# Performance work log

Hardware: AMD Instinct MI355X
Metric: run time of the kernel (lower is better)

## Reference

```python
import jax, jax.numpy as jnp
import numpy as np

NUM_ITERS = 3     # args.num_iters_sk
EPSILON = 0.05    # args.epsilon_sk
# imb_factor = 1 -> uniform row marginal r

B, K = 16384, 4096  # batch, num prototypes/classes


def setup_inputs() -> dict:
    key = jax.random.key(0)
    logits = jax.random.normal(key, (B, K), dtype=jnp.float32)
    return {"logits": logits}


def shoot_infs(x):
    # Replace infs by the max of the tensor with infs zeroed (matches torch helper)
    mask = jnp.isinf(x)
    tmp = jnp.where(mask, jnp.zeros((), x.dtype), x)
    m = jnp.max(tmp)
    return jnp.where(mask, m, tmp)


def reference(logits):
    q = logits / EPSILON
    q = q - jnp.max(q)          # global max for numerical stability
    Q = jnp.exp(q).T            # [K, B]
    Q = shoot_infs(Q)
    Q = Q / jnp.sum(Q)
    k, b = Q.shape
    r = jnp.full((k,), 1.0 / k, dtype=Q.dtype)  # uniform class marginal (imb_factor == 1)
    c = jnp.full((b,), 1.0 / b, dtype=Q.dtype)  # uniform sample marginal
    for _ in range(NUM_ITERS):
        u = r / jnp.sum(Q, axis=1)
        u = shoot_infs(u)
        Q = Q * u[:, None]
        Q = Q * (c / jnp.sum(Q, axis=0))[None, :]
    return (Q / jnp.sum(Q, axis=0, keepdims=True)).T.astype(jnp.float32)  # [B, K]
```

## Files before the change

### kernel.cpp

```cpp
#include <hip/hip_runtime.h>
#include <hip/hip_bf16.h>
#include <math.h>

#define EPS_INV 20.0f
#define B_ROWS 16384
#define K_COLS 4096

__device__ __forceinline__ unsigned enc_f(float f) {
  unsigned u = __float_as_uint(f);
  return (u & 0x80000000u) ? ~u : (u | 0x80000000u);
}
__device__ __forceinline__ float dec_f(unsigned u) {
  u = (u & 0x80000000u) ? (u ^ 0x80000000u) : ~u;
  return __uint_as_float(u);
}

__global__ void k_max(const float4* __restrict__ x, unsigned* __restrict__ gmax, int n4) {
  int tid = blockIdx.x * blockDim.x + threadIdx.x;
  int stride = gridDim.x * blockDim.x;
  float m = -3.4e38f;
  for (int i = tid; i < n4; i += stride) {
    float4 v = x[i];
    m = fmaxf(m, fmaxf(fmaxf(v.x, v.y), fmaxf(v.z, v.w)));
  }
  #pragma unroll
  for (int off = 32; off > 0; off >>= 1)
    m = fmaxf(m, __shfl_xor(m, off, 64));
  if ((threadIdx.x & 63) == 0) atomicMax(gmax, enc_f(m));
}

__global__ void k_colsum(const float* __restrict__ logits,
                         const unsigned* __restrict__ gmaxp,
                         const float* __restrict__ beta,
                         float* __restrict__ T, int rows_per_block) {
  float m = dec_f(*gmaxp);
  int c0 = blockIdx.x * 1024 + threadIdx.x * 4;
  int r0 = blockIdx.y * rows_per_block;
  float4 acc = make_float4(0.f, 0.f, 0.f, 0.f);
  for (int r = r0; r < r0 + rows_per_block; ++r) {
    float w = beta ? beta[r] : 1.0f;
    float4 v = *(const float4*)(logits + (size_t)r * K_COLS + c0);
    acc.x += w * __expf((v.x - m) * EPS_INV);
    acc.y += w * __expf((v.y - m) * EPS_INV);
    acc.z += w * __expf((v.z - m) * EPS_INV);
    acc.w += w * __expf((v.w - m) * EPS_INV);
  }
  atomicAdd(T + c0 + 0, acc.x);
  atomicAdd(T + c0 + 1, acc.y);
  atomicAdd(T + c0 + 2, acc.z);
  atomicAdd(T + c0 + 3, acc.w);
}

__global__ void k_alpha1(const float* __restrict__ T0, float* __restrict__ alpha) {
  __shared__ float sred[4];
  int tid = threadIdx.x;
  float s = 0.f;
  for (int i = tid; i < K_COLS; i += 256) s += T0[i];
  #pragma unroll
  for (int off = 32; off > 0; off >>= 1) s += __shfl_xor(s, off, 64);
  if ((tid & 63) == 0) sred[tid >> 6] = s;
  __syncthreads();
  float S = sred[0] + sred[1] + sred[2] + sred[3];
  float c = S * (1.0f / (float)K_COLS);
  for (int i = tid; i < K_COLS; i += 256) alpha[i] = c / T0[i];
}

__global__ void k_alpha_from_T(const float* __restrict__ T, float* __restrict__ alpha) {
  int i = blockIdx.x * blockDim.x + threadIdx.x;
  if (i < K_COLS) alpha[i] = (1.0f / (float)K_COLS) / T[i];
}

__global__ void k_rowsum_beta(const float* __restrict__ logits,
                              const unsigned* __restrict__ gmaxp,
                              const float* __restrict__ alpha,
                              float* __restrict__ beta) {
  float m = dec_f(*gmaxp);
  int lane = threadIdx.x & 63;
  int r = blockIdx.x * 4 + (threadIdx.x >> 6);
  const float4* row = (const float4*)(logits + (size_t)r * K_COLS);
  const float4* a4 = (const float4*)alpha;
  float acc = 0.f;
  #pragma unroll
  for (int j = 0; j < 16; ++j) {
    int i = lane + j * 64;
    float4 v = row[i];
    float4 a = a4[i];
    acc += a.x * __expf((v.x - m) * EPS_INV)
         + a.y * __expf((v.y - m) * EPS_INV)
         + a.z * __expf((v.z - m) * EPS_INV)
         + a.w * __expf((v.w - m) * EPS_INV);
  }
  #pragma unroll
  for (int off = 32; off > 0; off >>= 1) acc += __shfl_xor(acc, off, 64);
  if (lane == 0) beta[r] = (1.0f / (float)B_ROWS) / acc;
}

__global__ void k_finalize(const float* __restrict__ logits,
                           const unsigned* __restrict__ gmaxp,
                           const float* __restrict__ alpha,
                           float4* __restrict__ out) {
  float m = dec_f(*gmaxp);
  int lane = threadIdx.x & 63;
  int r = blockIdx.x * 4 + (threadIdx.x >> 6);
  const float4* row = (const float4*)(logits + (size_t)r * K_COLS);
  const float4* a4 = (const float4*)alpha;
  float4 prod[16];
  float acc = 0.f;
  #pragma unroll
  for (int j = 0; j < 16; ++j) {
    int i = lane + j * 64;
    float4 v = row[i];
    float4 a = a4[i];
    float4 p;
    p.x = a.x * __expf((v.x - m) * EPS_INV);
    p.y = a.y * __expf((v.y - m) * EPS_INV);
    p.z = a.z * __expf((v.z - m) * EPS_INV);
    p.w = a.w * __expf((v.w - m) * EPS_INV);
    prod[j] = p;
    acc += p.x + p.y + p.z + p.w;
  }
  #pragma unroll
  for (int off = 32; off > 0; off >>= 1) acc += __shfl_xor(acc, off, 64);
  float inv = 1.0f / acc;
  float4* orow = out + (size_t)r * (K_COLS / 4);
  #pragma unroll
  for (int j = 0; j < 16; ++j) {
    int i = lane + j * 64;
    float4 p = prod[j];
    p.x *= inv; p.y *= inv; p.z *= inv; p.w *= inv;
    orow[i] = p;
  }
}

extern "C" void kernel_launch(void* const* d_in, const int* in_sizes, int n_in,
                              void* d_out, int out_size, void* d_ws, size_t ws_size,
                              hipStream_t stream) {
  const float* logits = (const float*)d_in[0];
  char* ws = (char*)d_ws;

  unsigned* gmax = (unsigned*)ws;
  float* T0    = (float*)(ws + 1024);
  float* T1    = T0 + K_COLS;
  float* T2    = T1 + K_COLS;
  float* alpha = T2 + K_COLS;
  float* beta  = alpha + K_COLS;

  hipMemsetAsync(d_ws, 0, 1024 + 3 * K_COLS * sizeof(float), stream);

  const int n4 = (B_ROWS * K_COLS) / 4;
  k_max<<<2048, 256, 0, stream>>>((const float4*)logits, gmax, n4);

  dim3 cs_grid(4, 256);
  k_colsum<<<cs_grid, 256, 0, stream>>>(logits, gmax, nullptr, T0, 64);
  k_alpha1<<<1, 256, 0, stream>>>(T0, alpha);

  k_rowsum_beta<<<B_ROWS / 4, 256, 0, stream>>>(logits, gmax, alpha, beta);
  k_colsum<<<cs_grid, 256, 0, stream>>>(logits, gmax, beta, T1, 64);
  k_alpha_from_T<<<K_COLS / 256, 256, 0, stream>>>(T1, alpha);

  k_rowsum_beta<<<B_ROWS / 4, 256, 0, stream>>>(logits, gmax, alpha, beta);
  k_colsum<<<cs_grid, 256, 0, stream>>>(logits, gmax, beta, T2, 64);
  k_alpha_from_T<<<K_COLS / 256, 256, 0, stream>>>(T2, alpha);

  k_finalize<<<B_ROWS / 4, 256, 0, stream>>>(logits, gmax, alpha, (float4*)d_out);
}
```

Baseline: 792.6 us.

## Cache exp values as bf16 and fuse row/column Sinkhorn passes

The first column-sum pass now also writes exp((x-m)/eps) as a bf16 matrix into the workspace. Later Sinkhorn iterations read that half-size matrix instead of recomputing exp from the fp32 logits, which cuts memory traffic and transcendental work. The rowsum and beta-weighted colsum are fused into one kernel that accumulates column sums in shared memory, removing one full pass per iteration. The max kernel is unrolled with more loads in flight. Rounding the intermediates to bf16 lowers accuracy, and the fast path needs a 128MB workspace, otherwise it falls back to fused fp32 kernels.

New measurement: 1.379 ms. 74.0% more time.

```diff
diff --git a/kernel.cpp b/kernel.cpp
--- a/kernel.cpp
+++ b/kernel.cpp
@@ -5,6 +5,7 @@
 #define EPS_INV 20.0f
 #define B_ROWS 16384
 #define K_COLS 4096
+#define N4     ((B_ROWS * (size_t)K_COLS) / 4)
 
 __device__ __forceinline__ unsigned enc_f(float f) {
   unsigned u = __float_as_uint(f);
@@ -15,40 +16,61 @@
   return __uint_as_float(u);
 }
 
-__global__ void k_max(const float4* __restrict__ x, unsigned* __restrict__ gmax, int n4) {
-  int tid = blockIdx.x * blockDim.x + threadIdx.x;
-  int stride = gridDim.x * blockDim.x;
+__device__ __forceinline__ unsigned short f2bf(float f) {
+  unsigned u = __float_as_uint(f);
+  return (unsigned short)((u + 0x7FFFu + ((u >> 16) & 1u)) >> 16);
+}
+__device__ __forceinline__ float bf_lo(unsigned w) { return __uint_as_float(w << 16); }
+__device__ __forceinline__ float bf_hi(unsigned w) { return __uint_as_float(w & 0xFFFF0000u); }
+
+__global__ __launch_bounds__(256) void k_max(const float4* __restrict__ x,
+                                             unsigned* __restrict__ gmax) {
+  const int tid = blockIdx.x * 256 + threadIdx.x;
+  const int nth = 1024 * 256;
   float m = -3.4e38f;
-  for (int i = tid; i < n4; i += stride) {
-    float4 v = x[i];
-    m = fmaxf(m, fmaxf(fmaxf(v.x, v.y), fmaxf(v.z, v.w)));
-  }
-  #pragma unroll
-  for (int off = 32; off > 0; off >>= 1)
-    m = fmaxf(m, __shfl_xor(m, off, 64));
+  for (int it = 0; it < 8; ++it) {
+    float4 v[8];
+    #pragma unroll
+    for (int j = 0; j < 8; ++j) v[j] = x[(size_t)tid + (size_t)(it * 8 + j) * nth];
+    #pragma unroll
+    for (int j = 0; j < 8; ++j)
+      m = fmaxf(m, fmaxf(fmaxf(v[j].x, v[j].y), fmaxf(v[j].z, v[j].w)));
+  }
+  #pragma unroll
+  for (int off = 32; off > 0; off >>= 1) m = fmaxf(m, __shfl_xor(m, off, 64));
   if ((threadIdx.x & 63) == 0) atomicMax(gmax, enc_f(m));
 }
 
-__global__ void k_colsum(const float* __restrict__ logits,
-                         const unsigned* __restrict__ gmaxp,
-                         const float* __restrict__ beta,
-                         float* __restrict__ T, int rows_per_block) {
-  float m = dec_f(*gmaxp);
-  int c0 = blockIdx.x * 1024 + threadIdx.x * 4;
-  int r0 = blockIdx.y * rows_per_block;
+__global__ __launch_bounds__(256) void k_exp_colsum(const float* __restrict__ logits,
+                                                    const unsigned* __restrict__ gmaxp,
+                                                    unsigned short* __restrict__ E,
+                                                    float* __restrict__ T0) {
+  const float m = dec_f(*gmaxp);
+  const int c0 = blockIdx.x * 1024 + threadIdx.x * 4;
+  const int r0 = blockIdx.y * 64;
   float4 acc = make_float4(0.f, 0.f, 0.f, 0.f);
-  for (int r = r0; r < r0 + rows_per_block; ++r) {
-    float w = beta ? beta[r] : 1.0f;
-    float4 v = *(const float4*)(logits + (size_t)r * K_COLS + c0);
-    acc.x += w * __expf((v.x - m) * EPS_INV);
-    acc.y += w * __expf((v.y - m) * EPS_INV);
-    acc.z += w * __expf((v.z - m) * EPS_INV);
-    acc.w += w * __expf((v.w - m) * EPS_INV);
-  }
-  atomicAdd(T + c0 + 0, acc.x);
-  atomicAdd(T + c0 + 1, acc.y);
-  atomicAdd(T + c0 + 2, acc.z);
-  atomicAdd(T + c0 + 3, acc.w);
+  for (int rr = 0; rr < 64; rr += 4) {
+    float4 v[4];
+    #pragma unroll
+    for (int j = 0; j < 4; ++j)
+      v[j] = *(const float4*)(logits + (size_t)(r0 + rr + j) * K_COLS + c0);
+    #pragma unroll
+    for (int j = 0; j < 4; ++j) {
+      float e0 = __expf((v[j].x - m) * EPS_INV);
+      float e1 = __expf((v[j].y - m) * EPS_INV);
+      float e2 = __expf((v[j].z - m) * EPS_INV);
+      float e3 = __expf((v[j].w - m) * EPS_INV);
+      acc.x += e0; acc.y += e1; acc.z += e2; acc.w += e3;
+      if (E) {
+        ushort4 w = make_ushort4(f2bf(e0), f2bf(e1), f2bf(e2), f2bf(e3));
+        *(ushort4*)(E + (size_t)(r0 + rr + j) * K_COLS + c0) = w;
+      }
+    }
+  }
+  atomicAdd(T0 + c0 + 0, acc.x);
+  atomicAdd(T0 + c0 + 1, acc.y);
+  atomicAdd(T0 + c0 + 2, acc.z);
+  atomicAdd(T0 + c0 + 3, acc.w);
 }
 
 __global__ void k_alpha1(const float* __restrict__ T0, float* __restrict__ alpha) {
@@ -70,54 +92,170 @@
   if (i < K_COLS) alpha[i] = (1.0f / (float)K_COLS) / T[i];
 }
 
-__global__ void k_rowsum_beta(const float* __restrict__ logits,
-                              const unsigned* __restrict__ gmaxp,
-                              const float* __restrict__ alpha,
-                              float* __restrict__ beta) {
-  float m = dec_f(*gmaxp);
-  int lane = threadIdx.x & 63;
-  int r = blockIdx.x * 4 + (threadIdx.x >> 6);
-  const float4* row = (const float4*)(logits + (size_t)r * K_COLS);
+__global__ __launch_bounds__(256) void k_fused_E(const unsigned* __restrict__ Epk,
+                                                 const float* __restrict__ alpha,
+                                                 float* __restrict__ T) {
+  __shared__ float sT[4096];
+  for (int i = threadIdx.x; i < 4096; i += 256) sT[i] = 0.f;
+  __syncthreads();
+  const int lane = threadIdx.x & 63;
+  const int widx = threadIdx.x >> 6;
   const float4* a4 = (const float4*)alpha;
-  float acc = 0.f;
-  #pragma unroll
-  for (int j = 0; j < 16; ++j) {
-    int i = lane + j * 64;
-    float4 v = row[i];
-    float4 a = a4[i];
-    acc += a.x * __expf((v.x - m) * EPS_INV)
-         + a.y * __expf((v.y - m) * EPS_INV)
-         + a.z * __expf((v.z - m) * EPS_INV)
-         + a.w * __expf((v.w - m) * EPS_INV);
-  }
-  #pragma unroll
-  for (int off = 32; off > 0; off >>= 1) acc += __shfl_xor(acc, off, 64);
-  if (lane == 0) beta[r] = (1.0f / (float)B_ROWS) / acc;
-}
-
-__global__ void k_finalize(const float* __restrict__ logits,
-                           const unsigned* __restrict__ gmaxp,
-                           const float* __restrict__ alpha,
-                           float4* __restrict__ out) {
-  float m = dec_f(*gmaxp);
-  int lane = threadIdx.x & 63;
-  int r = blockIdx.x * 4 + (threadIdx.x >> 6);
+  const int r0 = blockIdx.x * 32 + widx * 8;
+  for (int rr = 0; rr < 8; ++rr) {
+    const int r = r0 + rr;
+    const uint4* e4 = (const uint4*)Epk + (size_t)r * 512;
+    uint4 ev[8];
+    #pragma unroll
+    for (int j = 0; j < 8; ++j) ev[j] = e4[lane + j * 64];
+    float s = 0.f;
+    #pragma unroll
+    for (int j = 0; j < 8; ++j) {
+      int cb = (lane + j * 64) * 2;
+      float4 a0 = a4[cb], a1 = a4[cb + 1];
+      s += a0.x * bf_lo(ev[j].x) + a0.y * bf_hi(ev[j].x)
+         + a0.z * bf_lo(ev[j].y) + a0.w * bf_hi(ev[j].y)
+         + a1.x * bf_lo(ev[j].z) + a1.y * bf_hi(ev[j].z)
+         + a1.z * bf_lo(ev[j].w) + a1.w * bf_hi(ev[j].w);
+    }
+    #pragma unroll
+    for (int off = 32; off > 0; off >>= 1) s += __shfl_xor(s, off, 64);
+    float beta = (1.0f / (float)B_ROWS) / s;
+    #pragma unroll
+    for (int j = 0; j < 8; ++j) {
+      int c = lane + j * 64;
+      atomicAdd(&sT[0 * 512 + c], beta * bf_lo(ev[j].x));
+      atomicAdd(&sT[1 * 512 + c], beta * bf_hi(ev[j].x));
+      atomicAdd(&sT[2 * 512 + c], beta * bf_lo(ev[j].y));
+      atomicAdd(&sT[3 * 512 + c], beta * bf_hi(ev[j].y));
+      atomicAdd(&sT[4 * 512 + c], beta * bf_lo(ev[j].z));
+      atomicAdd(&sT[5 * 512 + c], beta * bf_hi(ev[j].z));
+      atomicAdd(&sT[6 * 512 + c], beta * bf_lo(ev[j].w));
+      atomicAdd(&sT[7 * 512 + c], beta * bf_hi(ev[j].w));
+    }
+  }
+  __syncthreads();
+  for (int i = threadIdx.x; i < 4096; i += 256) {
+    int col = ((i & 511) << 3) | (i >> 9);
+    atomicAdd(T + col, sT[i]);
+  }
+}
+
+__global__ __launch_bounds__(256) void k_finalize_E(const unsigned* __restrict__ Epk,
+                                                    const float* __restrict__ alpha,
+                                                    float4* __restrict__ out) {
+  const int lane = threadIdx.x & 63;
+  const int r = blockIdx.x * 4 + (threadIdx.x >> 6);
+  const uint4* e4 = (const uint4*)Epk + (size_t)r * 512;
+  const float4* a4 = (const float4*)alpha;
+  uint4 ev[8];
+  #pragma unroll
+  for (int j = 0; j < 8; ++j) ev[j] = e4[lane + j * 64];
+  float s = 0.f;
+  #pragma unroll
+  for (int j = 0; j < 8; ++j) {
+    int cb = (lane + j * 64) * 2;
+    float4 a0 = a4[cb], a1 = a4[cb + 1];
+    s += a0.x * bf_lo(ev[j].x) + a0.y * bf_hi(ev[j].x)
+       + a0.z * bf_lo(ev[j].y) + a0.w * bf_hi(ev[j].y)
+       + a1.x * bf_lo(ev[j].z) + a1.y * bf_hi(ev[j].z)
+       + a1.z * bf_lo(ev[j].w) + a1.w * bf_hi(ev[j].w);
+  }
+  #pragma unroll
+  for (int off = 32; off > 0; off >>= 1) s += __shfl_xor(s, off, 64);
+  float inv = 1.0f / s;
+  float4* orow = out + (size_t)r * (K_COLS / 4);
+  #pragma unroll
+  for (int j = 0; j < 8; ++j) {
+    int cb = (lane + j * 64) * 2;
+    float4 a0 = a4[cb], a1 = a4[cb + 1];
+    float4 o0, o1;
+    o0.x = a0.x * bf_lo(ev[j].x) * inv;  o0.y = a0.y * bf_hi(ev[j].x) * inv;
+    o0.z = a0.z * bf_lo(ev[j].y) * inv;  o0.w = a0.w * bf_hi(ev[j].y) * inv;
+    o1.x = a1.x * bf_lo(ev[j].z) * inv;  o1.y = a1.y * bf_hi(ev[j].z) * inv;
+    o1.z = a1.z * bf_lo(ev[j].w) * inv;  o1.w = a1.w * bf_hi(ev[j].w) * inv;
+    orow[cb] = o0;
+    orow[cb + 1] = o1;
+  }
+}
+
+__global__ __launch_bounds__(256) void k_fused_L(const float* __restrict__ logits,
+                                                 const unsigned* __restrict__ gmaxp,
+                                                 const float* __restrict__ alpha,
+                                                 float* __restrict__ T) {
+  __shared__ float sT[4096];
+  for (int i = threadIdx.x; i < 4096; i += 256) sT[i] = 0.f;
+  __syncthreads();
+  const float m = dec_f(*gmaxp);
+  const int lane = threadIdx.x & 63;
+  const int widx = threadIdx.x >> 6;
+  const float4* a4 = (const float4*)alpha;
+  const int r0 = blockIdx.x * 32 + widx * 8;
+  for (int rr = 0; rr < 8; ++rr) {
+    const int r = r0 + rr;
+    const float4* row = (const float4*)(logits + (size_t)r * K_COLS);
+    float s = 0.f;
+    for (int h = 0; h < 2; ++h) {
+      float4 v[8];
+      #pragma unroll
+      for (int j = 0; j < 8; ++j) v[j] = row[lane + (h * 8 + j) * 64];
+      #pragma unroll
+      for (int j = 0; j < 8; ++j) {
+        float4 a = a4[lane + (h * 8 + j) * 64];
+        s += a.x * __expf((v[j].x - m) * EPS_INV) + a.y * __expf((v[j].y - m) * EPS_INV)
+           + a.z * __expf((v[j].z - m) * EPS_INV) + a.w * __expf((v[j].w - m) * EPS_INV);
+      }
+    }
+    #pragma unroll
+    for (int off = 32; off > 0; off >>= 1) s += __shfl_xor(s, off, 64);
+    float beta = (1.0f / (float)B_ROWS) / s;
+    for (int h = 0; h < 2; ++h) {
+      float4 v[8];
+      #pragma unroll
+      for (int j = 0; j < 8; ++j) v[j] = row[lane + (h * 8 + j) * 64];
+      #pragma unroll
+      for (int j = 0; j < 8; ++j) {
+        int c = lane + (h * 8 + j) * 64;
+        atomicAdd(&sT[0 * 1024 + c], beta * __expf((v[j].x - m) * EPS_INV));
+        atomicAdd(&sT[1 * 1024 + c], beta * __expf((v[j].y - m) * EPS_INV));
+        atomicAdd(&sT[2 * 1024 + c], beta * __expf((v[j].z - m) * EPS_INV));
+        atomicAdd(&sT[3 * 1024 + c], beta * __expf((v[j].w - m) * EPS_INV));
+      }
+    }
+  }
+  __syncthreads();
+  for (int i = threadIdx.x; i < 4096; i += 256) {
+    int col = ((i & 1023) << 2) | (i >> 10);
+    atomicAdd(T + col, sT[i]);
+  }
+}
+
+__global__ __launch_bounds__(256) void k_finalize_L(const float* __restrict__ logits,
+                                                    const unsigned* __restrict__ gmaxp,
+                                                    const float* __restrict__ alpha,
+                                                    float4* __restrict__ out) {
+  const float m = dec_f(*gmaxp);
+  const int lane = threadIdx.x & 63;
+  const int r = blockIdx.x * 4 + (threadIdx.x >> 6);
   const float4* row = (const float4*)(logits + (size_t)r * K_COLS);
   const float4* a4 = (const float4*)alpha;
   float4 prod[16];
   float acc = 0.f;
-  #pragma unroll
-  for (int j = 0; j < 16; ++j) {
-    int i = lane + j * 64;
-    float4 v = row[i];
-    float4 a = a4[i];
-    float4 p;
-    p.x = a.x * __expf((v.x - m) * EPS_INV);
-    p.y = a.y * __expf((v.y - m) * EPS_INV);
-    p.z = a.z * __expf((v.z - m) * EPS_INV);
-    p.w = a.w * __expf((v.w - m) * EPS_INV);
-    prod[j] = p;
-    acc += p.x + p.y + p.z + p.w;
+  for (int h = 0; h < 4; ++h) {
+    float4 v[4];
+    #pragma unroll
+    for (int j = 0; j < 4; ++j) v[j] = row[lane + (h * 4 + j) * 64];
+    #pragma unroll
+    for (int j = 0; j < 4; ++j) {
+      float4 a = a4[lane + (h * 4 + j) * 64];
+      float4 p;
+      p.x = a.x * __expf((v[j].x - m) * EPS_INV);
+      p.y = a.y * __expf((v[j].y - m) * EPS_INV);
+      p.z = a.z * __expf((v[j].z - m) * EPS_INV);
+      p.w = a.w * __expf((v[j].w - m) * EPS_INV);
+      prod[h * 4 + j] = p;
+      acc += p.x + p.y + p.z + p.w;
+    }
   }
   #pragma unroll
   for (int off = 32; off > 0; off >>= 1) acc += __shfl_xor(acc, off, 64);
@@ -125,10 +263,9 @@
   float4* orow = out + (size_t)r * (K_COLS / 4);
   #pragma unroll
   for (int j = 0; j < 16; ++j) {
-    int i = lane + j * 64;
     float4 p = prod[j];
     p.x *= inv; p.y *= inv; p.z *= inv; p.w *= inv;
-    orow[i] = p;
+    orow[lane + j * 64] = p;
   }
 }
 
@@ -140,27 +277,33 @@
 
   unsigned* gmax = (unsigned*)ws;
   float* T0    = (float*)(ws + 1024);
-  float* T1    = T0 + K_COLS;
-  float* T2    = T1 + K_COLS;
-  float* alpha = T2 + K_COLS;
-  float* beta  = alpha + K_COLS;
-
-  hipMemsetAsync(d_ws, 0, 1024 + 3 * K_COLS * sizeof(float), stream);
-
-  const int n4 = (B_ROWS * K_COLS) / 4;
-  k_max<<<2048, 256, 0, stream>>>((const float4*)logits, gmax, n4);
+  float* T1    = (float*)(ws + 17408);
+  float* T2    = (float*)(ws + 33792);
+  float* alpha = (float*)(ws + 50176);
+  unsigned short* E = (unsigned short*)(ws + (1 << 20));
+  const size_t need_bigws = (1ull << 20) + 2ull * B_ROWS * K_COLS;
+  const bool bigws = ws_size >= need_bigws;
+
+  hipMemsetAsync(d_ws, 0, 50176, stream);
+
+  k_max<<<1024, 256, 0, stream>>>((const float4*)logits, gmax);
 
   dim3 cs_grid(4, 256);
-  k_colsum<<<cs_grid, 256, 0, stream>>>(logits, gmax, nullptr, T0, 64);
-  k_alpha1<<<1, 256, 0, stream>>>(T0, alpha);
-
-  k_rowsum_beta<<<B_ROWS / 4, 256, 0, stream>>>(logits, gmax, alpha, beta);
-  k_colsum<<<cs_grid, 256, 0, stream>>>(logits, gmax, beta, T1, 64);
-  k_alpha_from_T<<<K_COLS / 256, 256, 0, stream>>>(T1, alpha);
-
-  k_rowsum_beta<<<B_ROWS / 4, 256, 0, stream>>>(logits, gmax, alpha, beta);
-  k_colsum<<<cs_grid, 256, 0, stream>>>(logits, gmax, beta, T2, 64);
-  k_alpha_from_T<<<K_COLS / 256, 256, 0, stream>>>(T2, alpha);
-
-  k_finalize<<<B_ROWS / 4, 256, 0, stream>>>(logits, gmax, alpha, (float4*)d_out);
-}
+  if (bigws) {
+    k_exp_colsum<<<cs_grid, 256, 0, stream>>>(logits, gmax, E, T0);
+    k_alpha1<<<1, 256, 0, stream>>>(T0, alpha);
+    k_fused_E<<<512, 256, 0, stream>>>((const unsigned*)E, alpha, T1);
+    k_alpha_from_T<<<K_COLS / 256, 256, 0, stream>>>(T1, alpha);
+    k_fused_E<<<512, 256, 0, stream>>>((const unsigned*)E, alpha, T2);
+    k_alpha_from_T<<<K_COLS / 256, 256, 0, stream>>>(T2, alpha);
+    k_finalize_E<<<B_ROWS / 4, 256, 0, stream>>>((const unsigned*)E, alpha, (float4*)d_out);
+  } else {
+    k_exp_colsum<<<cs_grid, 256, 0, stream>>>(logits, gmax, nullptr, T0);
+    k_alpha1<<<1, 256, 0, stream>>>(T0, alpha);
+    k_fused_L<<<512, 256, 0, stream>>>(logits, gmax, alpha, T1);
+    k_alpha_from_T<<<K_COLS / 256, 256, 0, stream>>>(T1, alpha);
+    k_fused_L<<<512, 256, 0, stream>>>(logits, gmax, alpha, T2);
+    k_alpha_from_T<<<K_COLS / 256, 256, 0, stream>>>(T2, alpha);
+    k_finalize_L<<<B_ROWS / 4, 256, 0, stream>>>(logits, gmax, alpha, (float4*)d_out);
+  }
+}
```
